# Kernel optimization log

Measured on AMD Instinct MI355X. Metric: run time of the kernel, lower is better.

## Reference

```python
import jax, jax.numpy as jnp
import numpy as np

N = 20000   # nodes
E = 320000  # edges (before self-loops)
D = 32      # num_hidden
H1 = 8      # heads layer 1
H2 = 1      # heads layer 2
NEG_SLOPE = 0.2  # PyG GATConv default


def setup_inputs() -> dict:
    key = jax.random.key(0)
    ks = jax.random.split(key, 12)
    features = jax.random.normal(ks[0], (N, D), jnp.float32)
    src = jax.random.randint(ks[1], (E,), 0, N, dtype=jnp.int32)
    dst = jax.random.randint(ks[2], (E,), 0, N, dtype=jnp.int32)
    dst = jnp.where(src == dst, (dst + 1) % N, dst)  # remove_self_loops equivalent
    edge_index = jnp.stack([src, dst])
    s = 0.1
    W1 = jax.random.normal(ks[3], (D, H1 * D), jnp.float32) * s
    att_src1 = jax.random.normal(ks[4], (1, H1, D), jnp.float32) * s
    att_dst1 = jax.random.normal(ks[5], (1, H1, D), jnp.float32) * s
    b1 = jnp.zeros((H1 * D,), jnp.float32)
    W2 = jax.random.normal(ks[6], (H1 * D, H2 * D), jnp.float32) * s
    att_src2 = jax.random.normal(ks[7], (1, H2, D), jnp.float32) * s
    att_dst2 = jax.random.normal(ks[8], (1, H2, D), jnp.float32) * s
    b2 = jnp.zeros((D,), jnp.float32)
    return {"features": features, "edge_index": edge_index,
            "W1": W1, "att_src1": att_src1, "att_dst1": att_dst1, "b1": b1,
            "W2": W2, "att_src2": att_src2, "att_dst2": att_dst2, "b2": b2}


def gat_conv(x, src, dst, W, a_src, a_dst, b, heads, out_c, concat):
    n = x.shape[0]
    xh = (x @ W).reshape(n, heads, out_c)              # [N,H,C]
    alpha_src = jnp.sum(xh * a_src, axis=-1)           # [N,H]
    alpha_dst = jnp.sum(xh * a_dst, axis=-1)           # [N,H]
    e = jax.nn.leaky_relu(alpha_src[src] + alpha_dst[dst], NEG_SLOPE)  # [Etot,H]
    # segment softmax over target node (dst); self-loops guarantee nonempty segments
    m = jax.lax.stop_gradient(jax.ops.segment_max(e, dst, num_segments=n))
    ex = jnp.exp(e - m[dst])
    denom = jax.ops.segment_sum(ex, dst, num_segments=n)
    alpha = ex / (denom[dst] + 1e-16)                  # [Etot,H]
    out = jax.ops.segment_sum(xh[src] * alpha[:, :, None], dst, num_segments=n)  # [N,H,C]
    out = out.reshape(n, heads * out_c) if concat else out.mean(axis=1)
    return out + b


def reference(features, edge_index, W1, att_src1, att_dst1, b1, W2, att_src2, att_dst2, b2):
    n = features.shape[0]
    loops = jnp.arange(n, dtype=edge_index.dtype)
    src = jnp.concatenate([edge_index[0], loops])
    dst = jnp.concatenate([edge_index[1], loops])
    x = jax.nn.relu(gat_conv(features, src, dst, W1, att_src1, att_dst1, b1, H1, D, True))
    # dropout is a no-op in eval mode
    out = gat_conv(x, src, dst, W2, att_src2, att_dst2, b2, H2, D, False)
    return out
```

## Files before the change

### kernel.cpp

```cpp
#include <hip/hip_runtime.h>
#include <hip/hip_bf16.h>

#define H1 8
#define F1 256
#define NEG 0.2f
#define DEGCAP 64
#define NPB 16

__global__ void scan_blk(int* __restrict__ counts, int N, int* __restrict__ bsum) {
    __shared__ int tmp[256];
    int tid = threadIdx.x;
    int i = blockIdx.x * 256 + tid;
    int v = (i < N) ? counts[i] : 0;
    tmp[tid] = v;
    __syncthreads();
    for (int off = 1; off < 256; off <<= 1) {
        int u = (tid >= off) ? tmp[tid - off] : 0;
        __syncthreads();
        tmp[tid] += u;
        __syncthreads();
    }
    if (i < N) counts[i] = tmp[tid] - v;
    if (tid == 255) bsum[blockIdx.x] = tmp[255];
}

__global__ void scan_add2(const int* __restrict__ excl, const int* __restrict__ bsum, int nb, int N,
                          int* __restrict__ rowptr, int* __restrict__ cursor) {
    __shared__ int sb[256];
    int tid = threadIdx.x, bid = blockIdx.x;
    int v = 0;
    if (tid < nb && (bid == 0 || tid < bid)) v = bsum[tid];
    sb[tid] = v;
    __syncthreads();
    for (int off = 128; off; off >>= 1) {
        if (tid < off) sb[tid] += sb[tid + off];
        __syncthreads();
    }
    int s0 = sb[0];
    int boff = (bid == 0) ? 0 : s0;
    if (bid == 0 && tid == 0) rowptr[N] = s0;
    int i = bid * 256 + tid;
    if (i < N) {
        int rp = excl[i] + boff;
        rowptr[i] = rp;
        cursor[i] = rp;
    }
}

__global__ void scatter_edges(const int* __restrict__ src_in, const int* __restrict__ dst_in,
                              int E, int N, int* __restrict__ cursor, int* __restrict__ csr_src) {
    int i = blockIdx.x * blockDim.x + threadIdx.x;
    int tot = E + N;
    if (i < tot) {
        int s, d;
        if (i < E) { s = src_in[i]; d = dst_in[i]; }
        else       { s = i - E;     d = i - E; }
        int pos = atomicAdd(&cursor[d], 1);
        csr_src[pos] = s;
    }
}

__global__ __launch_bounds__(256) void count_alpha(
    const int* __restrict__ dst_in, int E, int N, int* __restrict__ counts, int CB,
    const float* __restrict__ x, const float* __restrict__ W1,
    const float* __restrict__ as1, const float* __restrict__ ad1,
    float* __restrict__ asrc, float* __restrict__ adst) {
    __shared__ float sws[8 * 33], swd[8 * 33];
    __shared__ float sx[32 * 33];
    if (blockIdx.x < CB) {
        int tot = E + N;
        for (int i = blockIdx.x * 256 + threadIdx.x; i < tot; i += CB * 256) {
            int d = (i < E) ? dst_in[i] : (i - E);
            atomicAdd(&counts[d], 1);
        }
        return;
    }
    int t = threadIdx.x;
    {
        int h = t >> 5, d = t & 31;
        float s1 = 0.f, d1 = 0.f;
#pragma unroll
        for (int c = 0; c < 32; ++c) {
            float w = W1[d * F1 + h * 32 + c];
            s1 = fmaf(w, as1[h * 32 + c], s1);
            d1 = fmaf(w, ad1[h * 32 + c], d1);
        }
        sws[h * 33 + d] = s1; swd[h * 33 + d] = d1;
    }
    int base = (blockIdx.x - CB) * 32;
    for (int i = t; i < 1024; i += 256) {
        int r = i >> 5, d = i & 31;
        int n = base + r;
        sx[r * 33 + d] = (n < N) ? x[n * 32 + d] : 0.f;
    }
    __syncthreads();
    int r = t >> 3, h = t & 7;
    float ps = 0.f, pd = 0.f;
#pragma unroll
    for (int d = 0; d < 32; ++d) {
        float xv = sx[r * 33 + d];
        ps = fmaf(xv, sws[h * 33 + d], ps);
        pd = fmaf(xv, swd[h * 33 + d], pd);
    }
    int n = base + r;
    if (n < N) { asrc[n * 8 + h] = ps; adst[n * 8 + h] = pd; }
}

__global__ __launch_bounds__(256) void agg1(
    const float* __restrict__ x, const float* __restrict__ asrc, const float* __restrict__ adst,
    const int* __restrict__ rowptr, const int* __restrict__ csr_src,
    float* __restrict__ AGG, int N) {
    __shared__ float sA[4][H1][68];
    __shared__ int   sS[4][DEGCAP];
    int tid = threadIdx.x;
    int w = tid >> 6;
    int lane = tid & 63;
    int node = blockIdx.x * 4 + w;
    if (node >= N) return;
    int beg = rowptr[node];
    int deg = rowptr[node + 1] - beg;

    if (deg <= DEGCAP) {
        bool vi = lane < deg;
        int s = vi ? csr_src[beg + lane] : 0;
        sS[w][lane] = s;
        float4 d0 = *reinterpret_cast<const float4*>(&adst[node * 8]);
        float4 d1 = *reinterpret_cast<const float4*>(&adst[node * 8 + 4]);
        float4 a0 = make_float4(0.f, 0.f, 0.f, 0.f), a1 = a0;
        if (vi) {
            a0 = *reinterpret_cast<const float4*>(&asrc[s * 8]);
            a1 = *reinterpret_cast<const float4*>(&asrc[s * 8 + 4]);
        }
        float e[8];
        e[0] = a0.x + d0.x; e[1] = a0.y + d0.y; e[2] = a0.z + d0.z; e[3] = a0.w + d0.w;
        e[4] = a1.x + d1.x; e[5] = a1.y + d1.y; e[6] = a1.z + d1.z; e[7] = a1.w + d1.w;
#pragma unroll
        for (int h = 0; h < 8; ++h) {
            float ev = fmaxf(e[h], NEG * e[h]);
            e[h] = vi ? ev : -1e30f;
        }
#pragma unroll
        for (int h = 0; h < 8; ++h) {
            float m = e[h];
#pragma unroll
            for (int off = 32; off; off >>= 1) m = fmaxf(m, __shfl_xor(m, off, 64));
            float wv = vi ? __expf(e[h] - m) : 0.f;
            float ssum = wv;
#pragma unroll
            for (int off = 32; off; off >>= 1) ssum += __shfl_xor(ssum, off, 64);
            sA[w][h][lane] = wv * (1.f / (ssum + 1e-16f));
        }
        int h = lane >> 3, cq = lane & 7;
        float ax = 0.f, ay = 0.f, az = 0.f, aw = 0.f;
        int degP = (deg + 7) & ~7;
        for (int j = 0; j < degP; j += 8) {
            int4   t0 = *reinterpret_cast<const int4*>(&sS[w][j]);
            int4   t1 = *reinterpret_cast<const int4*>(&sS[w][j + 4]);
            float4 l0 = *reinterpret_cast<const float4*>(&sA[w][h][j]);
            float4 l1 = *reinterpret_cast<const float4*>(&sA[w][h][j + 4]);
            float4 v0 = *reinterpret_cast<const float4*>(&x[t0.x * 32 + cq * 4]);
            float4 v1 = *reinterpret_cast<const float4*>(&x[t0.y * 32 + cq * 4]);
            float4 v2 = *reinterpret_cast<const float4*>(&x[t0.z * 32 + cq * 4]);
            float4 v3 = *reinterpret_cast<const float4*>(&x[t0.w * 32 + cq * 4]);
            float4 u0 = *reinterpret_cast<const float4*>(&x[t1.x * 32 + cq * 4]);
            float4 u1 = *reinterpret_cast<const float4*>(&x[t1.y * 32 + cq * 4]);
            float4 u2 = *reinterpret_cast<const float4*>(&x[t1.z * 32 + cq * 4]);
            float4 u3 = *reinterpret_cast<const float4*>(&x[t1.w * 32 + cq * 4]);
            ax = fmaf(l0.x, v0.x, ax); ay = fmaf(l0.x, v0.y, ay); az = fmaf(l0.x, v0.z, az); aw = fmaf(l0.x, v0.w, aw);
            ax = fmaf(l0.y, v1.x, ax); ay = fmaf(l0.y, v1.y, ay); az = fmaf(l0.y, v1.z, az); aw = fmaf(l0.y, v1.w, aw);
            ax = fmaf(l0.z, v2.x, ax); ay = fmaf(l0.z, v2.y, ay); az = fmaf(l0.z, v2.z, az); aw = fmaf(l0.z, v2.w, aw);
            ax = fmaf(l0.w, v3.x, ax); ay = fmaf(l0.w, v3.y, ay); az = fmaf(l0.w, v3.z, az); aw = fmaf(l0.w, v3.w, aw);
            ax = fmaf(l1.x, u0.x, ax); ay = fmaf(l1.x, u0.y, ay); az = fmaf(l1.x, u0.z, az); aw = fmaf(l1.x, u0.w, aw);
            ax = fmaf(l1.y, u1.x, ax); ay = fmaf(l1.y, u1.y, ay); az = fmaf(l1.y, u1.z, az); aw = fmaf(l1.y, u1.w, aw);
            ax = fmaf(l1.z, u2.x, ax); ay = fmaf(l1.z, u2.y, ay); az = fmaf(l1.z, u2.z, az); aw = fmaf(l1.z, u2.w, aw);
            ax = fmaf(l1.w, u3.x, ax); ay = fmaf(l1.w, u3.y, ay); az = fmaf(l1.w, u3.z, az); aw = fmaf(l1.w, u3.w, aw);
        }
        float4 o; o.x = ax; o.y = ay; o.z = az; o.w = aw;
        *reinterpret_cast<float4*>(&AGG[(size_t)node * F1 + h * 32 + cq * 4]) = o;
    } else {
        int h = lane >> 3, cq = lane & 7;
        float adn = adst[node * 8 + h];
        float m = -1e30f;
        for (int i = 0; i < deg; ++i) {
            int s = csr_src[beg + i];
            float e = asrc[s * 8 + h] + adn;
            e = fmaxf(e, NEG * e);
            m = fmaxf(m, e);
        }
        float dsum = 0.f;
        for (int i = 0; i < deg; ++i) {
            int s = csr_src[beg + i];
            float e = asrc[s * 8 + h] + adn;
            e = fmaxf(e, NEG * e);
            dsum += __expf(e - m);
        }
        float inv = 1.f / (dsum + 1e-16f);
        float ax = 0.f, ay = 0.f, az = 0.f, aw = 0.f;
        for (int i = 0; i < deg; ++i) {
            int s = csr_src[beg + i];
            float e = asrc[s * 8 + h] + adn;
            e = fmaxf(e, NEG * e);
            float a = __expf(e - m) * inv;
            float4 v = *reinterpret_cast<const float4*>(&x[s * 32 + cq * 4]);
            ax = fmaf(a, v.x, ax); ay = fmaf(a, v.y, ay); az = fmaf(a, v.z, az); aw = fmaf(a, v.w, aw);
        }
        float4 o; o.x = ax; o.y = ay; o.z = az; o.w = aw;
        *reinterpret_cast<float4*>(&AGG[(size_t)node * F1 + h * 32 + cq * 4]) = o;
    }
}

__global__ __launch_bounds__(256) void mlp(
    const float* __restrict__ AGG, const float* __restrict__ W1, const float* __restrict__ b1,
    const float* __restrict__ W2, const float* __restrict__ as2, const float* __restrict__ ad2,
    float* __restrict__ xh2, float* __restrict__ asrc2, float* __restrict__ adst2, int N) {
    __shared__ float sT[NPB][F1];
    __shared__ float spart[NPB][8][32];
    int tid = threadIdx.x;
    int h = tid >> 5, c = tid & 31;
    int base = blockIdx.x * NPB;

    for (int i = tid; i < NPB * (F1 / 4); i += 256) {
        int n = i >> 6, j = i & 63;
        float4 v = (base + n < N) ? reinterpret_cast<const float4*>(AGG)[(size_t)(base + n) * 64 + j]
                                  : make_float4(0.f, 0.f, 0.f, 0.f);
        reinterpret_cast<float4*>(&sT[n][0])[j] = v;
    }
    float w1r[32];
#pragma unroll
    for (int d = 0; d < 32; ++d) w1r[d] = W1[d * F1 + tid];
    float bb = b1[tid];
    __syncthreads();

    float x2r[NPB];
#pragma unroll
    for (int n = 0; n < NPB; ++n) {
        float v = 0.f;
#pragma unroll
        for (int j = 0; j < 8; ++j) {
            float4 a4 = *reinterpret_cast<const float4*>(&sT[n][h * 32 + 4 * j]);
            v = fmaf(a4.x, w1r[4 * j],     v);
            v = fmaf(a4.y, w1r[4 * j + 1], v);
            v = fmaf(a4.z, w1r[4 * j + 2], v);
            v = fmaf(a4.w, w1r[4 * j + 3], v);
        }
        x2r[n] = fmaxf(v + bb, 0.f);
    }
    __syncthreads();
#pragma unroll
    for (int n = 0; n < NPB; ++n) sT[n][tid] = x2r[n];
    float w2r[32];
#pragma unroll
    for (int k2 = 0; k2 < 32; ++k2) w2r[k2] = W2[(h * 32 + k2) * 32 + c];
    __syncthreads();

#pragma unroll
    for (int n = 0; n < NPB; ++n) {
        float p = 0.f;
#pragma unroll
        for (int j = 0; j < 8; ++j) {
            float4 a4 = *reinterpret_cast<const float4*>(&sT[n][h * 32 + 4 * j]);
            p = fmaf(a4.x, w2r[4 * j],     p);
            p = fmaf(a4.y, w2r[4 * j + 1], p);
            p = fmaf(a4.z, w2r[4 * j + 2], p);
            p = fmaf(a4.w, w2r[4 * j + 3], p);
        }
        spart[n][h][c] = p;
    }
    __syncthreads();

#pragma unroll
    for (int rep = 0; rep < 2; ++rep) {
        int n = (tid >> 5) + 8 * rep;
        float o = 0.f;
#pragma unroll
        for (int q = 0; q < 8; ++q) o += spart[n][q][c];
        int node = base + n;
        float ps = o * as2[c], pd = o * ad2[c];
#pragma unroll
        for (int off = 16; off; off >>= 1) { ps += __shfl_xor(ps, off, 32); pd += __shfl_xor(pd, off, 32); }
        if (node < N) {
            xh2[(size_t)node * 32 + c] = o;
            if (c == 0) { asrc2[node] = ps; adst2[node] = pd; }
        }
    }
}

__global__ __launch_bounds__(256) void agg2(
    const float* __restrict__ xh2, const float* __restrict__ asrc2, const float* __restrict__ adst2,
    const int* __restrict__ rowptr, const int* __restrict__ csr_src,
    const float* __restrict__ b2, float* __restrict__ out, int N) {
    __shared__ float sA[8][DEGCAP];
    __shared__ int   sS[8][DEGCAP];
    int tid = threadIdx.x;
    int g = tid >> 5, lane = tid & 31;
    int node = blockIdx.x * 8 + g;
    if (node >= N) return;
    int beg = rowptr[node];
    int deg = rowptr[node + 1] - beg;
    float adn = adst2[node];
    float acc = 0.f;
    if (deg <= DEGCAP) {
        int i0 = lane, i1 = 32 + lane;
        int s0 = (i0 < deg) ? csr_src[beg + i0] : 0;
        int s1 = (i1 < deg) ? csr_src[beg + i1] : 0;
        sS[g][i0] = s0;
        sS[g][i1] = s1;
        float e0 = -1e30f, e1 = -1e30f;
        if (i0 < deg) { e0 = asrc2[s0] + adn; e0 = fmaxf(e0, NEG * e0); }
        if (i1 < deg) { e1 = asrc2[s1] + adn; e1 = fmaxf(e1, NEG * e1); }
        float m = fmaxf(e0, e1);
#pragma unroll
        for (int off = 16; off; off >>= 1) m = fmaxf(m, __shfl_xor(m, off, 32));
        float w0 = (i0 < deg) ? __expf(e0 - m) : 0.f;
        float w1 = (i1 < deg) ? __expf(e1 - m) : 0.f;
        sA[g][i0] = w0;
        sA[g][i1] = w1;
        float dsum = w0 + w1;
#pragma unroll
        for (int off = 16; off; off >>= 1) dsum += __shfl_xor(dsum, off, 32);
        float inv = 1.f / (dsum + 1e-16f);
        int degP = (deg + 7) & ~7;
        float acc0 = 0.f, acc1 = 0.f, acc2 = 0.f, acc3 = 0.f;
        for (int i = 0; i < degP; i += 8) {
            int4   t0 = *reinterpret_cast<const int4*>(&sS[g][i]);
            int4   t1 = *reinterpret_cast<const int4*>(&sS[g][i + 4]);
            float4 a0 = *reinterpret_cast<const float4*>(&sA[g][i]);
            float4 a1 = *reinterpret_cast<const float4*>(&sA[g][i + 4]);
            acc0 = fmaf(a0.x, xh2[t0.x * 32 + lane], acc0);
            acc1 = fmaf(a0.y, xh2[t0.y * 32 + lane], acc1);
            acc2 = fmaf(a0.z, xh2[t0.z * 32 + lane], acc2);
            acc3 = fmaf(a0.w, xh2[t0.w * 32 + lane], acc3);
            acc0 = fmaf(a1.x, xh2[t1.x * 32 + lane], acc0);
            acc1 = fmaf(a1.y, xh2[t1.y * 32 + lane], acc1);
            acc2 = fmaf(a1.z, xh2[t1.z * 32 + lane], acc2);
            acc3 = fmaf(a1.w, xh2[t1.w * 32 + lane], acc3);
        }
        acc = ((acc0 + acc1) + (acc2 + acc3)) * inv;
    } else {
        float m = -1e30f;
        for (int i = lane; i < deg; i += 32) {
            int s = csr_src[beg + i];
            float e = asrc2[s] + adn;
            e = fmaxf(e, NEG * e);
            m = fmaxf(m, e);
        }
#pragma unroll
        for (int off = 16; off; off >>= 1) m = fmaxf(m, __shfl_xor(m, off, 32));
        float dsum = 0.f;
        for (int i = lane; i < deg; i += 32) {
            int s = csr_src[beg + i];
            float e = asrc2[s] + adn;
            e = fmaxf(e, NEG * e);
            dsum += __expf(e - m);
        }
#pragma unroll
        for (int off = 16; off; off >>= 1) dsum += __shfl_xor(dsum, off, 32);
        float inv = 1.f / (dsum + 1e-16f);
        for (int i = 0; i < deg; ++i) {
            int s = csr_src[beg + i];
            float e = asrc2[s] + adn;
            e = fmaxf(e, NEG * e);
            acc = fmaf(__expf(e - m) * inv, xh2[s * 32 + lane], acc);
        }
    }
    out[(size_t)node * 32 + lane] = acc + b2[lane];
}

extern "C" void kernel_launch(void* const* d_in, const int* in_sizes, int n_in,
                              void* d_out, int out_size, void* d_ws, size_t ws_size,
                              hipStream_t stream) {
    const float* features = (const float*)d_in[0];
    const int*   edge_idx = (const int*)d_in[1];
    const float* W1       = (const float*)d_in[2];
    const float* att_src1 = (const float*)d_in[3];
    const float* att_dst1 = (const float*)d_in[4];
    const float* b1       = (const float*)d_in[5];
    const float* W2       = (const float*)d_in[6];
    const float* att_src2 = (const float*)d_in[7];
    const float* att_dst2 = (const float*)d_in[8];
    const float* b2       = (const float*)d_in[9];
    float* out = (float*)d_out;

    const int N = in_sizes[0] / 32;
    const int E = in_sizes[1] / 2;
    const int Etot = E + N;
    const int nb = (N + 255) / 256;
    const int CB = 625;
    const int AB = (N + 31) / 32;
    const int* src_in = edge_idx;
    const int* dst_in = edge_idx + E;

    float* AGG   = (float*)d_ws;
    float* asrc1 = AGG + (size_t)N * F1;
    float* adst1 = asrc1 + (size_t)N * 8;
    float* xh2   = adst1 + (size_t)N * 8;
    float* asrc2 = xh2 + (size_t)N * 32;
    float* adst2 = asrc2 + N;
    int* rowptr  = (int*)(adst2 + N);
    int* cursor  = rowptr + (N + 1);
    int* counts  = cursor + N;
    int* bsum    = counts + N;
    int* csr_src = bsum + 128;

    hipMemsetAsync(counts, 0, (size_t)N * sizeof(int), stream);
    count_alpha<<<CB + AB, 256, 0, stream>>>(dst_in, E, N, counts, CB,
                                             features, W1, att_src1, att_dst1, asrc1, adst1);
    scan_blk<<<nb, 256, 0, stream>>>(counts, N, bsum);
    scan_add2<<<nb, 256, 0, stream>>>(counts, bsum, nb, N, rowptr, cursor);
    scatter_edges<<<(Etot + 255) / 256, 256, 0, stream>>>(src_in, dst_in, E, N, cursor, csr_src);

    agg1<<<(N + 3) / 4, 256, 0, stream>>>(features, asrc1, adst1, rowptr, csr_src, AGG, N);

    mlp<<<(N + NPB - 1) / NPB, 256, 0, stream>>>(AGG, W1, b1, W2, att_src2, att_dst2,
                                                 xh2, asrc2, adst2, N);

    agg2<<<(N + 7) / 8, 256, 0, stream>>>(xh2, asrc2, adst2, rowptr, csr_src, b2, out, N);
}
```

Before: 183.9 us.

## Fuse two-pass scan into decoupled lookback scan and software-pipeline gather loops

Replaces the two-kernel block scan plus offset-add with a single kernel that does a decoupled lookback over per-block descriptors, removing one launch and the round trip through global memory. The memset now also zeroes the descriptor array. The gather loops in both aggregation kernels are software-pipelined so the next eight neighbor rows are loaded while the current ones are accumulated, to hide gather latency. The lookback spin-waits on predecessor blocks, which relies on blocks being scheduled in order. With only 79 blocks this should be safe, and the pipelining adds register pressure.

```diff
diff --git a/kernel.cpp b/kernel.cpp
--- a/kernel.cpp
+++ b/kernel.cpp
@@ -7,10 +7,13 @@
 #define DEGCAP 64
 #define NPB 16
 
-__global__ void scan_blk(int* __restrict__ counts, int N, int* __restrict__ bsum) {
+__global__ void scan_lookback(const int* __restrict__ counts, int N,
+                              unsigned long long* __restrict__ descr,
+                              int* __restrict__ rowptr, int* __restrict__ cursor) {
     __shared__ int tmp[256];
-    int tid = threadIdx.x;
-    int i = blockIdx.x * 256 + tid;
+    __shared__ int s_pref;
+    int tid = threadIdx.x, b = blockIdx.x;
+    int i = b * 256 + tid;
     int v = (i < N) ? counts[i] : 0;
     tmp[tid] = v;
     __syncthreads();
@@ -20,31 +23,27 @@
         tmp[tid] += u;
         __syncthreads();
     }
-    if (i < N) counts[i] = tmp[tid] - v;
-    if (tid == 255) bsum[blockIdx.x] = tmp[255];
-}
-
-__global__ void scan_add2(const int* __restrict__ excl, const int* __restrict__ bsum, int nb, int N,
-                          int* __restrict__ rowptr, int* __restrict__ cursor) {
-    __shared__ int sb[256];
-    int tid = threadIdx.x, bid = blockIdx.x;
-    int v = 0;
-    if (tid < nb && (bid == 0 || tid < bid)) v = bsum[tid];
-    sb[tid] = v;
-    __syncthreads();
-    for (int off = 128; off; off >>= 1) {
-        if (tid < off) sb[tid] += sb[tid + off];
-        __syncthreads();
-    }
-    int s0 = sb[0];
-    int boff = (bid == 0) ? 0 : s0;
-    if (bid == 0 && tid == 0) rowptr[N] = s0;
-    int i = bid * 256 + tid;
+    int aggv = tmp[255];
+    if (tid == 0) {
+        atomicExch(&descr[b], (1ULL << 32) | (unsigned long long)(unsigned int)aggv);
+        int pref = 0;
+        for (int p = b - 1; p >= 0; --p) {
+            unsigned long long d;
+            do { d = atomicAdd(&descr[p], 0ULL); } while ((d >> 32) == 0ULL);
+            pref += (int)(unsigned int)d;
+            if ((d >> 32) == 2ULL) break;
+        }
+        atomicExch(&descr[b], (2ULL << 32) | (unsigned long long)(unsigned int)(pref + aggv));
+        s_pref = pref;
+    }
+    __syncthreads();
+    int pref = s_pref;
     if (i < N) {
-        int rp = excl[i] + boff;
+        int rp = tmp[tid] - v + pref;
         rowptr[i] = rp;
         cursor[i] = rp;
     }
+    if (b == gridDim.x - 1 && tid == 255) rowptr[N] = pref + aggv;
 }
 
 __global__ void scatter_edges(const int* __restrict__ src_in, const int* __restrict__ dst_in,
@@ -153,28 +152,50 @@
         int h = lane >> 3, cq = lane & 7;
         float ax = 0.f, ay = 0.f, az = 0.f, aw = 0.f;
         int degP = (deg + 7) & ~7;
-        for (int j = 0; j < degP; j += 8) {
-            int4   t0 = *reinterpret_cast<const int4*>(&sS[w][j]);
-            int4   t1 = *reinterpret_cast<const int4*>(&sS[w][j + 4]);
-            float4 l0 = *reinterpret_cast<const float4*>(&sA[w][h][j]);
-            float4 l1 = *reinterpret_cast<const float4*>(&sA[w][h][j + 4]);
-            float4 v0 = *reinterpret_cast<const float4*>(&x[t0.x * 32 + cq * 4]);
-            float4 v1 = *reinterpret_cast<const float4*>(&x[t0.y * 32 + cq * 4]);
-            float4 v2 = *reinterpret_cast<const float4*>(&x[t0.z * 32 + cq * 4]);
-            float4 v3 = *reinterpret_cast<const float4*>(&x[t0.w * 32 + cq * 4]);
-            float4 u0 = *reinterpret_cast<const float4*>(&x[t1.x * 32 + cq * 4]);
-            float4 u1 = *reinterpret_cast<const float4*>(&x[t1.y * 32 + cq * 4]);
-            float4 u2 = *reinterpret_cast<const float4*>(&x[t1.z * 32 + cq * 4]);
-            float4 u3 = *reinterpret_cast<const float4*>(&x[t1.w * 32 + cq * 4]);
-            ax = fmaf(l0.x, v0.x, ax); ay = fmaf(l0.x, v0.y, ay); az = fmaf(l0.x, v0.z, az); aw = fmaf(l0.x, v0.w, aw);
-            ax = fmaf(l0.y, v1.x, ax); ay = fmaf(l0.y, v1.y, ay); az = fmaf(l0.y, v1.z, az); aw = fmaf(l0.y, v1.w, aw);
-            ax = fmaf(l0.z, v2.x, ax); ay = fmaf(l0.z, v2.y, ay); az = fmaf(l0.z, v2.z, az); aw = fmaf(l0.z, v2.w, aw);
-            ax = fmaf(l0.w, v3.x, ax); ay = fmaf(l0.w, v3.y, ay); az = fmaf(l0.w, v3.z, az); aw = fmaf(l0.w, v3.w, aw);
-            ax = fmaf(l1.x, u0.x, ax); ay = fmaf(l1.x, u0.y, ay); az = fmaf(l1.x, u0.z, az); aw = fmaf(l1.x, u0.w, aw);
-            ax = fmaf(l1.y, u1.x, ax); ay = fmaf(l1.y, u1.y, ay); az = fmaf(l1.y, u1.z, az); aw = fmaf(l1.y, u1.w, aw);
-            ax = fmaf(l1.z, u2.x, ax); ay = fmaf(l1.z, u2.y, ay); az = fmaf(l1.z, u2.z, az); aw = fmaf(l1.z, u2.w, aw);
-            ax = fmaf(l1.w, u3.x, ax); ay = fmaf(l1.w, u3.y, ay); az = fmaf(l1.w, u3.z, az); aw = fmaf(l1.w, u3.w, aw);
-        }
+        float4 L0 = *reinterpret_cast<const float4*>(&sA[w][h][0]);
+        float4 L1 = *reinterpret_cast<const float4*>(&sA[w][h][4]);
+        int4   T0 = *reinterpret_cast<const int4*>(&sS[w][0]);
+        int4   T1 = *reinterpret_cast<const int4*>(&sS[w][4]);
+        float4 v0 = *reinterpret_cast<const float4*>(&x[T0.x * 32 + cq * 4]);
+        float4 v1 = *reinterpret_cast<const float4*>(&x[T0.y * 32 + cq * 4]);
+        float4 v2 = *reinterpret_cast<const float4*>(&x[T0.z * 32 + cq * 4]);
+        float4 v3 = *reinterpret_cast<const float4*>(&x[T0.w * 32 + cq * 4]);
+        float4 v4 = *reinterpret_cast<const float4*>(&x[T1.x * 32 + cq * 4]);
+        float4 v5 = *reinterpret_cast<const float4*>(&x[T1.y * 32 + cq * 4]);
+        float4 v6 = *reinterpret_cast<const float4*>(&x[T1.z * 32 + cq * 4]);
+        float4 v7 = *reinterpret_cast<const float4*>(&x[T1.w * 32 + cq * 4]);
+        for (int j = 8; j < degP; j += 8) {
+            float4 nL0 = *reinterpret_cast<const float4*>(&sA[w][h][j]);
+            float4 nL1 = *reinterpret_cast<const float4*>(&sA[w][h][j + 4]);
+            int4   nT0 = *reinterpret_cast<const int4*>(&sS[w][j]);
+            int4   nT1 = *reinterpret_cast<const int4*>(&sS[w][j + 4]);
+            float4 u0 = *reinterpret_cast<const float4*>(&x[nT0.x * 32 + cq * 4]);
+            float4 u1 = *reinterpret_cast<const float4*>(&x[nT0.y * 32 + cq * 4]);
+            float4 u2 = *reinterpret_cast<const float4*>(&x[nT0.z * 32 + cq * 4]);
+            float4 u3 = *reinterpret_cast<const float4*>(&x[nT0.w * 32 + cq * 4]);
+            float4 u4 = *reinterpret_cast<const float4*>(&x[nT1.x * 32 + cq * 4]);
+            float4 u5 = *reinterpret_cast<const float4*>(&x[nT1.y * 32 + cq * 4]);
+            float4 u6 = *reinterpret_cast<const float4*>(&x[nT1.z * 32 + cq * 4]);
+            float4 u7 = *reinterpret_cast<const float4*>(&x[nT1.w * 32 + cq * 4]);
+            ax = fmaf(L0.x, v0.x, ax); ay = fmaf(L0.x, v0.y, ay); az = fmaf(L0.x, v0.z, az); aw = fmaf(L0.x, v0.w, aw);
+            ax = fmaf(L0.y, v1.x, ax); ay = fmaf(L0.y, v1.y, ay); az = fmaf(L0.y, v1.z, az); aw = fmaf(L0.y, v1.w, aw);
+            ax = fmaf(L0.z, v2.x, ax); ay = fmaf(L0.z, v2.y, ay); az = fmaf(L0.z, v2.z, az); aw = fmaf(L0.z, v2.w, aw);
+            ax = fmaf(L0.w, v3.x, ax); ay = fmaf(L0.w, v3.y, ay); az = fmaf(L0.w, v3.z, az); aw = fmaf(L0.w, v3.w, aw);
+            ax = fmaf(L1.x, v4.x, ax); ay = fmaf(L1.x, v4.y, ay); az = fmaf(L1.x, v4.z, az); aw = fmaf(L1.x, v4.w, aw);
+            ax = fmaf(L1.y, v5.x, ax); ay = fmaf(L1.y, v5.y, ay); az = fmaf(L1.y, v5.z, az); aw = fmaf(L1.y, v5.w, aw);
+            ax = fmaf(L1.z, v6.x, ax); ay = fmaf(L1.z, v6.y, ay); az = fmaf(L1.z, v6.z, az); aw = fmaf(L1.z, v6.w, aw);
+            ax = fmaf(L1.w, v7.x, ax); ay = fmaf(L1.w, v7.y, ay); az = fmaf(L1.w, v7.z, az); aw = fmaf(L1.w, v7.w, aw);
+            L0 = nL0; L1 = nL1;
+            v0 = u0; v1 = u1; v2 = u2; v3 = u3; v4 = u4; v5 = u5; v6 = u6; v7 = u7;
+        }
+        ax = fmaf(L0.x, v0.x, ax); ay = fmaf(L0.x, v0.y, ay); az = fmaf(L0.x, v0.z, az); aw = fmaf(L0.x, v0.w, aw);
+        ax = fmaf(L0.y, v1.x, ax); ay = fmaf(L0.y, v1.y, ay); az = fmaf(L0.y, v1.z, az); aw = fmaf(L0.y, v1.w, aw);
+        ax = fmaf(L0.z, v2.x, ax); ay = fmaf(L0.z, v2.y, ay); az = fmaf(L0.z, v2.z, az); aw = fmaf(L0.z, v2.w, aw);
+        ax = fmaf(L0.w, v3.x, ax); ay = fmaf(L0.w, v3.y, ay); az = fmaf(L0.w, v3.z, az); aw = fmaf(L0.w, v3.w, aw);
+        ax = fmaf(L1.x, v4.x, ax); ay = fmaf(L1.x, v4.y, ay); az = fmaf(L1.x, v4.z, az); aw = fmaf(L1.x, v4.w, aw);
+        ax = fmaf(L1.y, v5.x, ax); ay = fmaf(L1.y, v5.y, ay); az = fmaf(L1.y, v5.z, az); aw = fmaf(L1.y, v5.w, aw);
+        ax = fmaf(L1.z, v6.x, ax); ay = fmaf(L1.z, v6.y, ay); az = fmaf(L1.z, v6.z, az); aw = fmaf(L1.z, v6.w, aw);
+        ax = fmaf(L1.w, v7.x, ax); ay = fmaf(L1.w, v7.y, ay); az = fmaf(L1.w, v7.z, az); aw = fmaf(L1.w, v7.w, aw);
         float4 o; o.x = ax; o.y = ay; o.z = az; o.w = aw;
         *reinterpret_cast<float4*>(&AGG[(size_t)node * F1 + h * 32 + cq * 4]) = o;
     } else {
@@ -321,20 +342,34 @@
         float inv = 1.f / (dsum + 1e-16f);
         int degP = (deg + 7) & ~7;
         float acc0 = 0.f, acc1 = 0.f, acc2 = 0.f, acc3 = 0.f;
-        for (int i = 0; i < degP; i += 8) {
-            int4   t0 = *reinterpret_cast<const int4*>(&sS[g][i]);
-            int4   t1 = *reinterpret_cast<const int4*>(&sS[g][i + 4]);
-            float4 a0 = *reinterpret_cast<const float4*>(&sA[g][i]);
-            float4 a1 = *reinterpret_cast<const float4*>(&sA[g][i + 4]);
-            acc0 = fmaf(a0.x, xh2[t0.x * 32 + lane], acc0);
-            acc1 = fmaf(a0.y, xh2[t0.y * 32 + lane], acc1);
-            acc2 = fmaf(a0.z, xh2[t0.z * 32 + lane], acc2);
-            acc3 = fmaf(a0.w, xh2[t0.w * 32 + lane], acc3);
-            acc0 = fmaf(a1.x, xh2[t1.x * 32 + lane], acc0);
-            acc1 = fmaf(a1.y, xh2[t1.y * 32 + lane], acc1);
-            acc2 = fmaf(a1.z, xh2[t1.z * 32 + lane], acc2);
-            acc3 = fmaf(a1.w, xh2[t1.w * 32 + lane], acc3);
-        }
+        float4 A0 = *reinterpret_cast<const float4*>(&sA[g][0]);
+        float4 A1 = *reinterpret_cast<const float4*>(&sA[g][4]);
+        int4   T0 = *reinterpret_cast<const int4*>(&sS[g][0]);
+        int4   T1 = *reinterpret_cast<const int4*>(&sS[g][4]);
+        float v0 = xh2[T0.x * 32 + lane], v1 = xh2[T0.y * 32 + lane];
+        float v2 = xh2[T0.z * 32 + lane], v3 = xh2[T0.w * 32 + lane];
+        float v4 = xh2[T1.x * 32 + lane], v5 = xh2[T1.y * 32 + lane];
+        float v6 = xh2[T1.z * 32 + lane], v7 = xh2[T1.w * 32 + lane];
+        for (int i = 8; i < degP; i += 8) {
+            float4 nA0 = *reinterpret_cast<const float4*>(&sA[g][i]);
+            float4 nA1 = *reinterpret_cast<const float4*>(&sA[g][i + 4]);
+            int4   nT0 = *reinterpret_cast<const int4*>(&sS[g][i]);
+            int4   nT1 = *reinterpret_cast<const int4*>(&sS[g][i + 4]);
+            float u0 = xh2[nT0.x * 32 + lane], u1 = xh2[nT0.y * 32 + lane];
+            float u2 = xh2[nT0.z * 32 + lane], u3 = xh2[nT0.w * 32 + lane];
+            float u4 = xh2[nT1.x * 32 + lane], u5 = xh2[nT1.y * 32 + lane];
+            float u6 = xh2[nT1.z * 32 + lane], u7 = xh2[nT1.w * 32 + lane];
+            acc0 = fmaf(A0.x, v0, acc0); acc1 = fmaf(A0.y, v1, acc1);
+            acc2 = fmaf(A0.z, v2, acc2); acc3 = fmaf(A0.w, v3, acc3);
+            acc0 = fmaf(A1.x, v4, acc0); acc1 = fmaf(A1.y, v5, acc1);
+            acc2 = fmaf(A1.z, v6, acc2); acc3 = fmaf(A1.w, v7, acc3);
+            A0 = nA0; A1 = nA1;
+            v0 = u0; v1 = u1; v2 = u2; v3 = u3; v4 = u4; v5 = u5; v6 = u6; v7 = u7;
+        }
+        acc0 = fmaf(A0.x, v0, acc0); acc1 = fmaf(A0.y, v1, acc1);
+        acc2 = fmaf(A0.z, v2, acc2); acc3 = fmaf(A0.w, v3, acc3);
+        acc0 = fmaf(A1.x, v4, acc0); acc1 = fmaf(A1.y, v5, acc1);
+        acc2 = fmaf(A1.z, v6, acc2); acc3 = fmaf(A1.w, v7, acc3);
         acc = ((acc0 + acc1) + (acc2 + acc3)) * inv;
     } else {
         float m = -1e30f;
@@ -397,16 +432,15 @@
     float* asrc2 = xh2 + (size_t)N * 32;
     float* adst2 = asrc2 + N;
     int* rowptr  = (int*)(adst2 + N);
-    int* cursor  = rowptr + (N + 1);
+    int* cursor  = rowptr + (N + 2);
     int* counts  = cursor + N;
-    int* bsum    = counts + N;
-    int* csr_src = bsum + 128;
-
-    hipMemsetAsync(counts, 0, (size_t)N * sizeof(int), stream);
+    unsigned long long* descr = (unsigned long long*)(counts + N);
+    int* csr_src = (int*)(descr + 128);
+
+    hipMemsetAsync(counts, 0, (size_t)(N + 256) * sizeof(int), stream);
     count_alpha<<<CB + AB, 256, 0, stream>>>(dst_in, E, N, counts, CB,
                                              features, W1, att_src1, att_dst1, asrc1, adst1);
-    scan_blk<<<nb, 256, 0, stream>>>(counts, N, bsum);
-    scan_add2<<<nb, 256, 0, stream>>>(counts, bsum, nb, N, rowptr, cursor);
+    scan_lookback<<<nb, 256, 0, stream>>>(counts, N, descr, rowptr, cursor);
     scatter_edges<<<(Etot + 255) / 256, 256, 0, stream>>>(src_in, dst_in, E, N, cursor, csr_src);
 
     agg1<<<(N + 3) / 4, 256, 0, stream>>>(features, asrc1, adst1, rowptr, csr_src, AGG, N);
```

New measurement: 189.0 us. 1.03x slower.

## Replace CSR build with fixed-capacity per-node buckets plus overflow list

Applied to the files above, without the earlier changes.

Removes the count/scan/scatter CSR construction (three kernels plus a second atomic pass) and instead scatters each edge directly into a fixed DEGCAP-slot bucket per destination node, with a global overflow list for high-degree nodes. The aggregation kernels read degree from the cursor array and source ids from the bucket. This cuts launches and one full pass over the edge list, at the cost of a larger sparse bucket array and a serial linear scan of the overflow list for nodes above the cap. The neighbor order inside a bucket is now nondeterministic, so floating-point summation order can vary between runs.

```diff
diff --git a/kernel.cpp b/kernel.cpp
--- a/kernel.cpp
+++ b/kernel.cpp
@@ -7,71 +7,23 @@
 #define DEGCAP 64
 #define NPB 16
 
-__global__ void scan_blk(int* __restrict__ counts, int N, int* __restrict__ bsum) {
-    __shared__ int tmp[256];
-    int tid = threadIdx.x;
-    int i = blockIdx.x * 256 + tid;
-    int v = (i < N) ? counts[i] : 0;
-    tmp[tid] = v;
-    __syncthreads();
-    for (int off = 1; off < 256; off <<= 1) {
-        int u = (tid >= off) ? tmp[tid - off] : 0;
-        __syncthreads();
-        tmp[tid] += u;
-        __syncthreads();
-    }
-    if (i < N) counts[i] = tmp[tid] - v;
-    if (tid == 255) bsum[blockIdx.x] = tmp[255];
-}
-
-__global__ void scan_add2(const int* __restrict__ excl, const int* __restrict__ bsum, int nb, int N,
-                          int* __restrict__ rowptr, int* __restrict__ cursor) {
-    __shared__ int sb[256];
-    int tid = threadIdx.x, bid = blockIdx.x;
-    int v = 0;
-    if (tid < nb && (bid == 0 || tid < bid)) v = bsum[tid];
-    sb[tid] = v;
-    __syncthreads();
-    for (int off = 128; off; off >>= 1) {
-        if (tid < off) sb[tid] += sb[tid + off];
-        __syncthreads();
-    }
-    int s0 = sb[0];
-    int boff = (bid == 0) ? 0 : s0;
-    if (bid == 0 && tid == 0) rowptr[N] = s0;
-    int i = bid * 256 + tid;
-    if (i < N) {
-        int rp = excl[i] + boff;
-        rowptr[i] = rp;
-        cursor[i] = rp;
-    }
-}
-
-__global__ void scatter_edges(const int* __restrict__ src_in, const int* __restrict__ dst_in,
-                              int E, int N, int* __restrict__ cursor, int* __restrict__ csr_src) {
-    int i = blockIdx.x * blockDim.x + threadIdx.x;
-    int tot = E + N;
-    if (i < tot) {
-        int s, d;
-        if (i < E) { s = src_in[i]; d = dst_in[i]; }
-        else       { s = i - E;     d = i - E; }
-        int pos = atomicAdd(&cursor[d], 1);
-        csr_src[pos] = s;
-    }
-}
-
-__global__ __launch_bounds__(256) void count_alpha(
-    const int* __restrict__ dst_in, int E, int N, int* __restrict__ counts, int CB,
+__global__ __launch_bounds__(256) void scatter_alpha(
+    const int* __restrict__ src_in, const int* __restrict__ dst_in, int E, int N, int SB,
+    int* __restrict__ cursor, int* __restrict__ bucket, int* __restrict__ ovf_cnt, int* __restrict__ ovf,
     const float* __restrict__ x, const float* __restrict__ W1,
     const float* __restrict__ as1, const float* __restrict__ ad1,
     float* __restrict__ asrc, float* __restrict__ adst) {
     __shared__ float sws[8 * 33], swd[8 * 33];
     __shared__ float sx[32 * 33];
-    if (blockIdx.x < CB) {
+    if (blockIdx.x < SB) {
         int tot = E + N;
-        for (int i = blockIdx.x * 256 + threadIdx.x; i < tot; i += CB * 256) {
-            int d = (i < E) ? dst_in[i] : (i - E);
-            atomicAdd(&counts[d], 1);
+        for (int i = blockIdx.x * 256 + threadIdx.x; i < tot; i += SB * 256) {
+            int s, d;
+            if (i < E) { s = src_in[i]; d = dst_in[i]; }
+            else       { s = i - E;     d = i - E; }
+            int pos = atomicAdd(&cursor[d], 1);
+            if (pos < DEGCAP) bucket[d * DEGCAP + pos] = s;
+            else { int o = atomicAdd(ovf_cnt, 1); ovf[2 * o] = s; ovf[2 * o + 1] = d; }
         }
         return;
     }
@@ -87,7 +39,7 @@
         }
         sws[h * 33 + d] = s1; swd[h * 33 + d] = d1;
     }
-    int base = (blockIdx.x - CB) * 32;
+    int base = (blockIdx.x - SB) * 32;
     for (int i = t; i < 1024; i += 256) {
         int r = i >> 5, d = i & 31;
         int n = base + r;
@@ -108,7 +60,8 @@
 
 __global__ __launch_bounds__(256) void agg1(
     const float* __restrict__ x, const float* __restrict__ asrc, const float* __restrict__ adst,
-    const int* __restrict__ rowptr, const int* __restrict__ csr_src,
+    const int* __restrict__ deg_arr, const int* __restrict__ bucket,
+    const int* __restrict__ ovf_cnt, const int* __restrict__ ovf,
     float* __restrict__ AGG, int N) {
     __shared__ float sA[4][H1][68];
     __shared__ int   sS[4][DEGCAP];
@@ -117,12 +70,12 @@
     int lane = tid & 63;
     int node = blockIdx.x * 4 + w;
     if (node >= N) return;
-    int beg = rowptr[node];
-    int deg = rowptr[node + 1] - beg;
+    int deg = deg_arr[node];
+    int bbase = node * DEGCAP;
 
     if (deg <= DEGCAP) {
         bool vi = lane < deg;
-        int s = vi ? csr_src[beg + lane] : 0;
+        int s = vi ? bucket[bbase + lane] : 0;
         sS[w][lane] = s;
         float4 d0 = *reinterpret_cast<const float4*>(&adst[node * 8]);
         float4 d1 = *reinterpret_cast<const float4*>(&adst[node * 8 + 4]);
@@ -180,24 +133,45 @@
     } else {
         int h = lane >> 3, cq = lane & 7;
         float adn = adst[node * 8 + h];
+        int oc = *ovf_cnt;
         float m = -1e30f;
-        for (int i = 0; i < deg; ++i) {
-            int s = csr_src[beg + i];
+        for (int i = 0; i < DEGCAP; ++i) {
+            int s = bucket[bbase + i];
             float e = asrc[s * 8 + h] + adn;
             e = fmaxf(e, NEG * e);
             m = fmaxf(m, e);
         }
+        for (int j = 0; j < oc; ++j) if (ovf[2 * j + 1] == node) {
+            int s = ovf[2 * j];
+            float e = asrc[s * 8 + h] + adn;
+            e = fmaxf(e, NEG * e);
+            m = fmaxf(m, e);
+        }
         float dsum = 0.f;
-        for (int i = 0; i < deg; ++i) {
-            int s = csr_src[beg + i];
+        for (int i = 0; i < DEGCAP; ++i) {
+            int s = bucket[bbase + i];
+            float e = asrc[s * 8 + h] + adn;
+            e = fmaxf(e, NEG * e);
+            dsum += __expf(e - m);
+        }
+        for (int j = 0; j < oc; ++j) if (ovf[2 * j + 1] == node) {
+            int s = ovf[2 * j];
             float e = asrc[s * 8 + h] + adn;
             e = fmaxf(e, NEG * e);
             dsum += __expf(e - m);
         }
         float inv = 1.f / (dsum + 1e-16f);
         float ax = 0.f, ay = 0.f, az = 0.f, aw = 0.f;
-        for (int i = 0; i < deg; ++i) {
-            int s = csr_src[beg + i];
+        for (int i = 0; i < DEGCAP; ++i) {
+            int s = bucket[bbase + i];
+            float e = asrc[s * 8 + h] + adn;
+            e = fmaxf(e, NEG * e);
+            float a = __expf(e - m) * inv;
+            float4 v = *reinterpret_cast<const float4*>(&x[s * 32 + cq * 4]);
+            ax = fmaf(a, v.x, ax); ay = fmaf(a, v.y, ay); az = fmaf(a, v.z, az); aw = fmaf(a, v.w, aw);
+        }
+        for (int j = 0; j < oc; ++j) if (ovf[2 * j + 1] == node) {
+            int s = ovf[2 * j];
             float e = asrc[s * 8 + h] + adn;
             e = fmaxf(e, NEG * e);
             float a = __expf(e - m) * inv;
@@ -287,7 +261,8 @@
 
 __global__ __launch_bounds__(256) void agg2(
     const float* __restrict__ xh2, const float* __restrict__ asrc2, const float* __restrict__ adst2,
-    const int* __restrict__ rowptr, const int* __restrict__ csr_src,
+    const int* __restrict__ deg_arr, const int* __restrict__ bucket,
+    const int* __restrict__ ovf_cnt, const int* __restrict__ ovf,
     const float* __restrict__ b2, float* __restrict__ out, int N) {
     __shared__ float sA[8][DEGCAP];
     __shared__ int   sS[8][DEGCAP];
@@ -295,14 +270,14 @@
     int g = tid >> 5, lane = tid & 31;
     int node = blockIdx.x * 8 + g;
     if (node >= N) return;
-    int beg = rowptr[node];
-    int deg = rowptr[node + 1] - beg;
+    int deg = deg_arr[node];
+    int bbase = node * DEGCAP;
     float adn = adst2[node];
     float acc = 0.f;
     if (deg <= DEGCAP) {
         int i0 = lane, i1 = 32 + lane;
-        int s0 = (i0 < deg) ? csr_src[beg + i0] : 0;
-        int s1 = (i1 < deg) ? csr_src[beg + i1] : 0;
+        int s0 = (i0 < deg) ? bucket[bbase + i0] : 0;
+        int s1 = (i1 < deg) ? bucket[bbase + i1] : 0;
         sS[g][i0] = s0;
         sS[g][i1] = s1;
         float e0 = -1e30f, e1 = -1e30f;
@@ -337,27 +312,42 @@
         }
         acc = ((acc0 + acc1) + (acc2 + acc3)) * inv;
     } else {
+        int oc = *ovf_cnt;
         float m = -1e30f;
-        for (int i = lane; i < deg; i += 32) {
-            int s = csr_src[beg + i];
+        for (int i = 0; i < DEGCAP; ++i) {
+            int s = bucket[bbase + i];
             float e = asrc2[s] + adn;
             e = fmaxf(e, NEG * e);
             m = fmaxf(m, e);
         }
-#pragma unroll
-        for (int off = 16; off; off >>= 1) m = fmaxf(m, __shfl_xor(m, off, 32));
+        for (int j = 0; j < oc; ++j) if (ovf[2 * j + 1] == node) {
+            int s = ovf[2 * j];
+            float e = asrc2[s] + adn;
+            e = fmaxf(e, NEG * e);
+            m = fmaxf(m, e);
+        }
         float dsum = 0.f;
-        for (int i = lane; i < deg; i += 32) {
-            int s = csr_src[beg + i];
+        for (int i = 0; i < DEGCAP; ++i) {
+            int s = bucket[bbase + i];
             float e = asrc2[s] + adn;
             e = fmaxf(e, NEG * e);
             dsum += __expf(e - m);
         }
-#pragma unroll
-        for (int off = 16; off; off >>= 1) dsum += __shfl_xor(dsum, off, 32);
+        for (int j = 0; j < oc; ++j) if (ovf[2 * j + 1] == node) {
+            int s = ovf[2 * j];
+            float e = asrc2[s] + adn;
+            e = fmaxf(e, NEG * e);
+            dsum += __expf(e - m);
+        }
         float inv = 1.f / (dsum + 1e-16f);
-        for (int i = 0; i < deg; ++i) {
-            int s = csr_src[beg + i];
+        for (int i = 0; i < DEGCAP; ++i) {
+            int s = bucket[bbase + i];
+            float e = asrc2[s] + adn;
+            e = fmaxf(e, NEG * e);
+            acc = fmaf(__expf(e - m) * inv, xh2[s * 32 + lane], acc);
+        }
+        for (int j = 0; j < oc; ++j) if (ovf[2 * j + 1] == node) {
+            int s = ovf[2 * j];
             float e = asrc2[s] + adn;
             e = fmaxf(e, NEG * e);
             acc = fmaf(__expf(e - m) * inv, xh2[s * 32 + lane], acc);
@@ -384,8 +374,7 @@
     const int N = in_sizes[0] / 32;
     const int E = in_sizes[1] / 2;
     const int Etot = E + N;
-    const int nb = (N + 255) / 256;
-    const int CB = 625;
+    const int SB = 672;
     const int AB = (N + 31) / 32;
     const int* src_in = edge_idx;
     const int* dst_in = edge_idx + E;
@@ -396,23 +385,20 @@
     float* xh2   = adst1 + (size_t)N * 8;
     float* asrc2 = xh2 + (size_t)N * 32;
     float* adst2 = asrc2 + N;
-    int* rowptr  = (int*)(adst2 + N);
-    int* cursor  = rowptr + (N + 1);
-    int* counts  = cursor + N;
-    int* bsum    = counts + N;
-    int* csr_src = bsum + 128;
-
-    hipMemsetAsync(counts, 0, (size_t)N * sizeof(int), stream);
-    count_alpha<<<CB + AB, 256, 0, stream>>>(dst_in, E, N, counts, CB,
-                                             features, W1, att_src1, att_dst1, asrc1, adst1);
-    scan_blk<<<nb, 256, 0, stream>>>(counts, N, bsum);
-    scan_add2<<<nb, 256, 0, stream>>>(counts, bsum, nb, N, rowptr, cursor);
-    scatter_edges<<<(Etot + 255) / 256, 256, 0, stream>>>(src_in, dst_in, E, N, cursor, csr_src);
-
-    agg1<<<(N + 3) / 4, 256, 0, stream>>>(features, asrc1, adst1, rowptr, csr_src, AGG, N);
+    int* cursor  = (int*)(adst2 + N);
+    int* ovf_cnt = cursor + N;
+    int* bucket  = ovf_cnt + 2;
+    int* ovf     = bucket + (size_t)N * DEGCAP;
+
+    hipMemsetAsync(cursor, 0, (size_t)(N + 2) * sizeof(int), stream);
+    scatter_alpha<<<SB + AB, 256, 0, stream>>>(src_in, dst_in, E, N, SB,
+                                               cursor, bucket, ovf_cnt, ovf,
+                                               features, W1, att_src1, att_dst1, asrc1, adst1);
+
+    agg1<<<(N + 3) / 4, 256, 0, stream>>>(features, asrc1, adst1, cursor, bucket, ovf_cnt, ovf, AGG, N);
 
     mlp<<<(N + NPB - 1) / NPB, 256, 0, stream>>>(AGG, W1, b1, W2, att_src2, att_dst2,
                                                  xh2, asrc2, adst2, N);
 
-    agg2<<<(N + 7) / 8, 256, 0, stream>>>(xh2, asrc2, adst2, rowptr, csr_src, b2, out, N);
+    agg2<<<(N + 7) / 8, 256, 0, stream>>>(xh2, asrc2, adst2, cursor, bucket, ovf_cnt, ovf, b2, out, N);
 }
```

After: 157.6 us. 14.3% less time.
